# Performance work log

Measured on AMD Instinct MI355X. Metric: run time of the kernel, lower is better.

## Reference

```python
import jax, jax.numpy as jnp
import numpy as np
from jax import lax

B, S, H, V, J, K = 8, 512, 768, 35004, 30, 9
PAD = 0

def setup_inputs() -> dict:
    key = jax.random.key(0)
    ks = jax.random.split(key, 12)
    std = 0.02
    return {
        'x': jax.random.randint(ks[0], (B, S), 0, V),
        'decoder_input': jax.random.normal(ks[1], (B, J, H), jnp.float32),
        'encoder_output': jax.random.normal(ks[2], (B, S, H), jnp.float32),
        'hidden': jax.random.normal(ks[3], (1, B, H), jnp.float32),
        'teacher': jax.random.randint(ks[4], (B, J, K), 0, V),
        'max_len': K,
        'embed': jax.random.normal(ks[5], (V, H), jnp.float32) * std,
        'w_ih': jax.random.normal(ks[6], (3 * H, H), jnp.float32) * std,
        'w_hh': jax.random.normal(ks[7], (3 * H, H), jnp.float32) * std,
        'b_ih': jnp.zeros((3 * H,), jnp.float32),
        'b_hh': jnp.zeros((3 * H,), jnp.float32),
        'wg_w': jax.random.normal(ks[8], (1, 3 * H), jnp.float32) * std,
        'wg_b': jnp.zeros((1,), jnp.float32),
    }

def gru_cell(w, h, w_ih, w_hh, b_ih, b_hh):
    # PyTorch GRU gate order: reset, update, new
    gi = w @ w_ih.T + b_ih          # [B,3H]
    gh = h @ w_hh.T + b_hh          # [B,3H]
    ir, iz, inn = jnp.split(gi, 3, axis=-1)
    hr, hz, hn = jnp.split(gh, 3, axis=-1)
    r = jax.nn.sigmoid(ir + hr)
    z = jax.nn.sigmoid(iz + hz)
    n = jnp.tanh(inn + r * hn)
    return (1.0 - z) * n + z * h

def reference(x, decoder_input, encoder_output, hidden, teacher, max_len,
              embed, w_ih, w_hh, b_ih, b_hh, wg_w, wg_b):
    mask = (x == PAD)                      # [B,S]
    batch_ix = jnp.arange(x.shape[0])[:, None]

    def tok_step(carry, teach_t):
        w, h = carry                       # w,h: [B,H]; teach_t: [B]
        h = gru_cell(w, h, w_ih, w_hh, b_ih, b_hh)
        logits_hist = jnp.einsum('bsh,bh->bs', encoder_output, h)
        logits_hist = jnp.where(mask, -1e9, logits_hist)
        a_hist = jax.nn.softmax(logits_hist, axis=-1)          # [B,S]
        a_vocab = jax.nn.softmax(h @ embed.T, axis=-1)         # [B,V]
        context = jnp.einsum('bs,bsh->bh', a_hist, encoder_output)
        p_gen = jax.nn.sigmoid(
            jnp.concatenate([w, h, context], axis=-1) @ wg_w.T + wg_b)  # [B,1]
        p_ctx = jnp.zeros_like(a_vocab).at[batch_ix, x].add(a_hist)     # scatter_add pointer copy
        p_final = p_gen * a_vocab + (1.0 - p_gen) * p_ctx
        w_next = embed[teach_t]            # teacher forcing (dropout omitted: eval mode)
        return (w_next, h), p_final

    def slot_step(h, slot_in):
        w0, teach_j = slot_in              # w0: [B,H]; teach_j: [K,B]
        (_, h), p = lax.scan(tok_step, (w0, h), teach_j)
        return h, p                        # p: [K,B,V]

    h0 = hidden[0]                                      # [B,H]
    slots = jnp.swapaxes(decoder_input, 0, 1)           # [J,B,H]
    teach = jnp.transpose(teacher, (1, 2, 0))           # [J,K,B]
    _, outs = lax.scan(slot_step, h0, (slots, teach))   # [J,K,B,V]
    return jnp.transpose(outs, (2, 0, 1, 3))            # [B,J,K,V]
```

## Files before the change

### kernel.cpp

```cpp
#include <hip/hip_runtime.h>
#include <hip/hip_bf16.h>

typedef _Float16 f16;
typedef _Float16 f16x8 __attribute__((ext_vector_type(8)));
typedef _Float16 f16x4v __attribute__((ext_vector_type(4)));
typedef _Float16 h2 __attribute__((ext_vector_type(2)));
typedef float f32x4 __attribute__((ext_vector_type(4)));
typedef unsigned ui4v __attribute__((ext_vector_type(4)));
typedef unsigned long long ull;

#define B_ 8
#define S_ 512
#define H_ 768
#define V_ 35004
#define J_ 30
#define K_ 9
#define R_ 2160
#define H3 2304
#define VMT 17
#define VNT 274


__global__ void k_zero(int* p, int n) {
    int i = blockIdx.x * 256 + threadIdx.x;
    if (i < n) p[i] = 0;
}

__global__ void k_cast(const float* __restrict__ s, f16* __restrict__ d, long n) {
    for (long i = (long)blockIdx.x * 256 + threadIdx.x; i < n; i += (long)gridDim.x * 256)
        d[i] = (f16)s[i];
}

__global__ void k_build_wall(const float* __restrict__ emb, const float* __restrict__ dec,
                             const int* __restrict__ teacher, f16* __restrict__ Wall) {
    int r = blockIdx.x;
    int b = r / 270, s = r % 270, j = s / 9, t = s % 9;
    const float* src = (t == 0) ? dec + ((long)b * J_ + j) * H_
                                : emb + (long)teacher[((long)b * J_ + j) * K_ + (t - 1)] * H_;
    f16* dst = Wall + (long)r * H_;
    for (int c = threadIdx.x; c < H_; c += 256) dst[c] = (f16)src[c];
}

__global__ void k_init_h(const float* __restrict__ hidden, ull* __restrict__ hbuf) {
    int i = blockIdx.x * 256 + threadIdx.x;
    if (i < B_ * H_) {
        int b = i / H_, u = i % H_;
        hbuf[(long)b * 1536 + u] = (ull)__float_as_uint(hidden[i]);
    }
}

typedef const __attribute__((address_space(1))) unsigned GASU;
typedef __attribute__((address_space(3))) unsigned LASU;
__device__ __forceinline__ void gld16(const f16* g, f16* l) {
    __builtin_amdgcn_global_load_lds((GASU*)g, (LASU*)l, 16, 0, 0);
}

template <int MODE>
__global__ __launch_bounds__(256) void k_gemm(const f16* __restrict__ A, const f16* __restrict__ Bm,
                                              float* __restrict__ C, const float* __restrict__ bias,
                                              int M, int N, int K, long sA, long sB, long sC) {
    A += (long)blockIdx.z * sA;
    Bm += (long)blockIdx.z * sB;
    C += (long)blockIdx.z * sC;
    const int m0 = blockIdx.y * 128, n0 = blockIdx.x * 128;
    __shared__ f16 As[128 * 32];
    __shared__ f16 Bs[128 * 32];
    const int tid = threadIdx.x, lane = tid & 63, wave = tid >> 6;
    const int wm = wave >> 1, wn = wave & 1;
    const int fr = lane & 15, kg = lane >> 4;
    f32x4 acc[4][4] = {};
    const int idxu = wave * 128;
    const int i0 = idxu + lane, i1 = idxu + 64 + lane;
    const int r0 = i0 >> 2, k80 = i0 & 3;
    const int r1 = i1 >> 2, k81 = i1 & 3;
    int ga0 = m0 + r0; if (ga0 >= M) ga0 = M - 1;
    int ga1 = m0 + r1; if (ga1 >= M) ga1 = M - 1;
    int gb0 = n0 + r0; if (gb0 >= N) gb0 = N - 1;
    int gb1 = n0 + r1; if (gb1 >= N) gb1 = N - 1;
    const f16* pa0 = A + (long)ga0 * K + k80 * 8;
    const f16* pa1 = A + (long)ga1 * K + k81 * 8;
    const f16* pb0 = Bm + (long)gb0 * K + k80 * 8;
    const f16* pb1 = Bm + (long)gb1 * K + k81 * 8;
    for (int kt = 0; kt < K; kt += 32) {
        gld16(pa0 + kt, As + idxu * 8);
        gld16(pa1 + kt, As + idxu * 8 + 512);
        gld16(pb0 + kt, Bs + idxu * 8);
        gld16(pb1 + kt, Bs + idxu * 8 + 512);
        __syncthreads();
        f16x8 af[4], bf[4];
#pragma unroll
        for (int m = 0; m < 4; ++m) af[m] = *(const f16x8*)(As + (wm * 64 + m * 16 + fr) * 32 + kg * 8);
#pragma unroll
        for (int n = 0; n < 4; ++n) bf[n] = *(const f16x8*)(Bs + (wn * 64 + n * 16 + fr) * 32 + kg * 8);
#pragma unroll
        for (int m = 0; m < 4; ++m)
#pragma unroll
            for (int n = 0; n < 4; ++n)
                acc[m][n] = __builtin_amdgcn_mfma_f32_16x16x32_f16(af[m], bf[n], acc[m][n], 0, 0, 0);
        __syncthreads();
    }
    const int crow = m0 + wm * 64 + (lane >> 4) * 4;
    const int ccol = n0 + wn * 64 + fr;
#pragma unroll
    for (int n = 0; n < 4; ++n) {
        int col = ccol + n * 16;
        if (col >= N) continue;
        float bv = (MODE == 1) ? bias[col] : 0.f;
#pragma unroll
        for (int m = 0; m < 4; ++m) {
#pragma unroll
            for (int q = 0; q < 4; ++q) {
                int row = crow + m * 16 + q;
                if (row < M) C[(long)row * N + col] = acc[m][n][q] + bv;
            }
        }
    }
}

__global__ __launch_bounds__(256) void k_attn3(const f16* __restrict__ Ahi, const f16* __restrict__ Alo,
                                               const f16* __restrict__ Bhi, const f16* __restrict__ Blo,
                                               float* __restrict__ C, int M, int N, int K,
                                               long sA, long sB, long sC) {
    const long za = (long)blockIdx.z * sA, zb = (long)blockIdx.z * sB;
    C += (long)blockIdx.z * sC;
    const int m0 = blockIdx.y * 128, n0 = blockIdx.x * 128;
    __shared__ f16 As[128 * 32];
    __shared__ f16 Bs[128 * 32];
    const int tid = threadIdx.x, lane = tid & 63, wave = tid >> 6;
    const int wm = wave >> 1, wn = wave & 1;
    const int fr = lane & 15, kg = lane >> 4;
    f32x4 acc[4][4] = {};
    const int idxu = wave * 128;
    const int i0 = idxu + lane, i1 = idxu + 64 + lane;
    const int r0 = i0 >> 2, k80 = i0 & 3;
    const int r1 = i1 >> 2, k81 = i1 & 3;
    int ga0 = m0 + r0; if (ga0 >= M) ga0 = M - 1;
    int ga1 = m0 + r1; if (ga1 >= M) ga1 = M - 1;
    int gb0 = n0 + r0; if (gb0 >= N) gb0 = N - 1;
    int gb1 = n0 + r1; if (gb1 >= N) gb1 = N - 1;
    const long oa0 = (long)ga0 * K + k80 * 8, oa1 = (long)ga1 * K + k81 * 8;
    const long ob0 = (long)gb0 * K + k80 * 8, ob1 = (long)gb1 * K + k81 * 8;
    for (int ph = 0; ph < 3; ++ph) {
        const f16* Ap = (ph == 2 ? Alo : Ahi) + za;
        const f16* Bp = (ph == 1 ? Blo : Bhi) + zb;
        for (int kt = 0; kt < K; kt += 32) {
            gld16(Ap + oa0 + kt, As + idxu * 8);
            gld16(Ap + oa1 + kt, As + idxu * 8 + 512);
            gld16(Bp + ob0 + kt, Bs + idxu * 8);
            gld16(Bp + ob1 + kt, Bs + idxu * 8 + 512);
            __syncthreads();
            f16x8 af[4], bf[4];
#pragma unroll
            for (int m = 0; m < 4; ++m) af[m] = *(const f16x8*)(As + (wm * 64 + m * 16 + fr) * 32 + kg * 8);
#pragma unroll
            for (int n = 0; n < 4; ++n) bf[n] = *(const f16x8*)(Bs + (wn * 64 + n * 16 + fr) * 32 + kg * 8);
#pragma unroll
            for (int m = 0; m < 4; ++m)
#pragma unroll
                for (int n = 0; n < 4; ++n)
                    acc[m][n] = __builtin_amdgcn_mfma_f32_16x16x32_f16(af[m], bf[n], acc[m][n], 0, 0, 0);
            __syncthreads();
        }
    }
    const int crow = m0 + wm * 64 + (lane >> 4) * 4;
    const int ccol = n0 + wn * 64 + fr;
#pragma unroll
    for (int n = 0; n < 4; ++n) {
        int col = ccol + n * 16;
        if (col >= N) continue;
#pragma unroll
        for (int m = 0; m < 4; ++m) {
#pragma unroll
            for (int q = 0; q < 4; ++q) {
                int row = crow + m * 16 + q;
                if (row < M) C[(long)row * N + col] = acc[m][n][q];
            }
        }
    }
}

__global__ __launch_bounds__(256) void k_vocab(const f16* __restrict__ A, const f16* __restrict__ Bm,
                                               float* __restrict__ C, float* __restrict__ psum) {
    const int M = R_, N = V_, K = H_;
    const int nwg = VMT * VNT;
    int lin = blockIdx.x;
    int q8 = nwg / 8, r8 = nwg % 8;
    int xcd = lin & 7, idx = lin >> 3;
    int newlin = (xcd < r8) ? xcd * (q8 + 1) + idx : r8 * (q8 + 1) + (xcd - r8) * q8 + idx;
    int mt = newlin % VMT, nt = newlin / VMT;
    const int m0 = mt * 128, n0 = nt * 128;
    __shared__ f16 As[128 * 32];
    __shared__ f16 Bs[128 * 32];
    __shared__ float rpart[2][128];
    const int tid = threadIdx.x, lane = tid & 63, wave = tid >> 6;
    const int wm = wave >> 1, wn = wave & 1;
    const int fr = lane & 15, kg = lane >> 4;
    f32x4 acc[4][4] = {};
    const int idxu = wave * 128;
    const int i0 = idxu + lane, i1 = idxu + 64 + lane;
    const int r0 = i0 >> 2, k80 = i0 & 3;
    const int r1 = i1 >> 2, k81 = i1 & 3;
    int ga0 = m0 + r0; if (ga0 >= M) ga0 = M - 1;
    int ga1 = m0 + r1; if (ga1 >= M) ga1 = M - 1;
    int gb0 = n0 + r0; if (gb0 >= N) gb0 = N - 1;
    int gb1 = n0 + r1; if (gb1 >= N) gb1 = N - 1;
    const f16* pa0 = A + (long)ga0 * K + k80 * 8;
    const f16* pa1 = A + (long)ga1 * K + k81 * 8;
    const f16* pb0 = Bm + (long)gb0 * K + k80 * 8;
    const f16* pb1 = Bm + (long)gb1 * K + k81 * 8;
    for (int kt = 0; kt < K; kt += 32) {
        gld16(pa0 + kt, As + idxu * 8);
        gld16(pa1 + kt, As + idxu * 8 + 512);
        gld16(pb0 + kt, Bs + idxu * 8);
        gld16(pb1 + kt, Bs + idxu * 8 + 512);
        __syncthreads();
        f16x8 af[4], bf[4];
#pragma unroll
        for (int m = 0; m < 4; ++m) af[m] = *(const f16x8*)(As + (wm * 64 + m * 16 + fr) * 32 + kg * 8);
#pragma unroll
        for (int n = 0; n < 4; ++n) bf[n] = *(const f16x8*)(Bs + (wn * 64 + n * 16 + fr) * 32 + kg * 8);
#pragma unroll
        for (int m = 0; m < 4; ++m)
#pragma unroll
            for (int n = 0; n < 4; ++n)
                acc[m][n] = __builtin_amdgcn_mfma_f32_16x16x32_f16(af[m], bf[n], acc[m][n], 0, 0, 0);
        __syncthreads();
    }
    const int crow = m0 + wm * 64 + (lane >> 4) * 4;
    const int ccol = n0 + wn * 64 + fr;
    float rs[4][4];
#pragma unroll
    for (int m = 0; m < 4; ++m)
#pragma unroll
        for (int q = 0; q < 4; ++q) rs[m][q] = 0.f;
#pragma unroll
    for (int n = 0; n < 4; ++n) {
        int col = ccol + n * 16;
        if (col >= N) continue;
#pragma unroll
        for (int m = 0; m < 4; ++m) {
#pragma unroll
            for (int q = 0; q < 4; ++q) {
                int row = crow + m * 16 + q;
                if (row < M) {
                    float e = __expf(acc[m][n][q]);
                    C[(long)row * N + col] = e;
                    rs[m][q] += e;
                }
            }
        }
    }
#pragma unroll
    for (int m = 0; m < 4; ++m)
#pragma unroll
        for (int q = 0; q < 4; ++q) {
            float v = rs[m][q];
            v += __shfl_xor(v, 1);
            v += __shfl_xor(v, 2);
            v += __shfl_xor(v, 4);
            v += __shfl_xor(v, 8);
            rs[m][q] = v;
        }
    if ((lane & 15) == 0) {
#pragma unroll
        for (int m = 0; m < 4; ++m)
#pragma unroll
            for (int q = 0; q < 4; ++q)
                rpart[wn][wm * 64 + (lane >> 4) * 4 + m * 16 + q] = rs[m][q];
    }
    __syncthreads();
    if (tid < 128) {
        int row = m0 + tid;
        if (row < M) psum[(long)nt * M + row] = rpart[0][tid] + rpart[1][tid];
    }
}

__device__ __forceinline__ float fd2(unsigned hv, unsigned wv, float acc) {
#if __has_builtin(__builtin_amdgcn_fdot2)
    return __builtin_amdgcn_fdot2(__builtin_bit_cast(h2, hv), __builtin_bit_cast(h2, wv), acc, false);
#else
    h2 a = __builtin_bit_cast(h2, hv), b = __builtin_bit_cast(h2, wv);
    return acc + (float)a.x * (float)b.x + (float)a.y * (float)b.y;
#endif
}

__global__ __launch_bounds__(256, 1) void k_gru(const float* __restrict__ gi,
                                                const float* __restrict__ whh,
                                                const float* __restrict__ bhh,
                                                ull* hbuf,
                                                f16* __restrict__ Hhi, f16* __restrict__ Hlo,
                                                const float* __restrict__ emb, f16* __restrict__ emb16,
                                                const float* __restrict__ enc, f16* __restrict__ ehi,
                                                f16* __restrict__ elo, f16* __restrict__ encT) {
    __shared__ ui4v wsvu[9216];
    __shared__ __align__(16) f16 hsf[768];
    __shared__ float part[2][8][32][3];
    const int tid = threadIdx.x;
    if (blockIdx.x >= 192) {
        const long pt = (long)(blockIdx.x - 192) * 256 + tid;
        const long n4 = (long)V_ * H_ / 4;
        for (long i = pt; i < n4; i += 64 * 256) {
            f32x4 v = ((const f32x4*)emb)[i];
            f16x4v r = {(f16)v.x, (f16)v.y, (f16)v.z, (f16)v.w};
            ((f16x4v*)emb16)[i] = r;
        }
        const long n4e = (long)B_ * S_ * H_ / 4;
        for (long i = pt; i < n4e; i += 64 * 256) {
            f32x4 v = ((const f32x4*)enc)[i];
            f16 h0 = (f16)v.x, h1 = (f16)v.y, h2v = (f16)v.z, h3 = (f16)v.w;
            f16x4v hv = {h0, h1, h2v, h3};
            ((f16x4v*)ehi)[i] = hv;
            f16x4v lv = {(f16)(v.x - (float)h0), (f16)(v.y - (float)h1),
                         (f16)(v.z - (float)h2v), (f16)(v.w - (float)h3)};
            ((f16x4v*)elo)[i] = lv;
        }
        float* tl = (float*)wsvu;
        for (int t = blockIdx.x - 192; t < 8 * 8 * 12; t += 64) {
            int ht = t % 12, st = (t / 12) % 8, bb = t / 96;
            __syncthreads();
#pragma unroll
            for (int k = 0; k < 16; ++k) {
                int i = tid + k * 256;
                int sl = i >> 6, hl = i & 63;
                tl[sl * 65 + hl] = enc[((long)bb * S_ + st * 64 + sl) * H_ + ht * 64 + hl];
            }
            __syncthreads();
#pragma unroll
            for (int k = 0; k < 16; ++k) {
                int i = tid + k * 256;
                int hl = i >> 6, sl = i & 63;
                encT[((long)bb * H_ + ht * 64 + hl) * S_ + st * 64 + sl] = (f16)tl[sl * 65 + hl];
            }
        }
        return;
    }
    const int chain = blockIdx.x / 24;
    const int blk = blockIdx.x % 24;
    const int u0 = blk * 32;
    for (int idx = tid; idx < 9216; idx += 256) {
        int uu = idx & 31, k8 = (idx >> 5) % 96, g = idx / (96 * 32);
        const float* src = whh + (long)(g * H_ + u0 + uu) * H_ + k8 * 8;
        f32x4 a = *(const f32x4*)src;
        f32x4 b2 = *(const f32x4*)(src + 4);
        f16x8 pk = {(f16)a.x, (f16)a.y, (f16)a.z, (f16)a.w,
                    (f16)b2.x, (f16)b2.y, (f16)b2.z, (f16)b2.w};
        wsvu[idx] = __builtin_bit_cast(ui4v, pk);
    }
    float b_r = 0.f, b_z = 0.f, b_n = 0.f;
    if (tid < 32) {
        int c = u0 + tid;
        b_r = bhh[c];
        b_z = bhh[H_ + c];
        b_n = bhh[2 * H_ + c];
    }
    __syncthreads();
    const int u = tid & 31, q = tid >> 5, lane = tid & 63;
    const int pw = (tid >> 6) * 192 + lane;
    ui4v wreg[3][12];
#pragma unroll
    for (int g = 0; g < 3; ++g)
#pragma unroll
        for (int i = 0; i < 12; ++i)
            wreg[g][i] = wsvu[(g * 96 + q * 12 + i) * 32 + u];
    ull* base = hbuf + (long)chain * 1536;
    const bool fin = (tid < 32);
    float g0 = 0.f, g1 = 0.f, g2v = 0.f;
    if (fin) {
        const float* gp = gi + (long)chain * 270 * H3;
        int c = u0 + tid;
        g0 = gp[c];
        g1 = gp[H_ + c];
        g2v = gp[2 * H_ + c];
    }
    for (int s = 0; s < 270; ++s) {
        const ull* rb = base + (s & 1) * 768;
        ull* wb = base + ((s + 1) & 1) * 768;
        const unsigned want = (unsigned)s;
        ull v0, v1, v2, vh = 0;
        for (;;) {
            v0 = __hip_atomic_load(rb + pw, __ATOMIC_RELAXED, __HIP_MEMORY_SCOPE_AGENT);
            v1 = __hip_atomic_load(rb + pw + 64, __ATOMIC_RELAXED, __HIP_MEMORY_SCOPE_AGENT);
            v2 = __hip_atomic_load(rb + pw + 128, __ATOMIC_RELAXED, __HIP_MEMORY_SCOPE_AGENT);
            bool ok = ((unsigned)(v0 >> 32) == want) & ((unsigned)(v1 >> 32) == want) &
                      ((unsigned)(v2 >> 32) == want);
            if (fin) {
                vh = __hip_atomic_load(rb + u0 + tid, __ATOMIC_RELAXED, __HIP_MEMORY_SCOPE_AGENT);
                ok &= ((unsigned)(vh >> 32) == want);
            }
            if (ok) break;
        }
        hsf[pw] = (f16)__uint_as_float((unsigned)v0);
        hsf[pw + 64] = (f16)__uint_as_float((unsigned)v1);
        hsf[pw + 128] = (f16)__uint_as_float((unsigned)v2);
        __builtin_amdgcn_wave_barrier();
        float ar = 0.f, az = 0.f, an = 0.f;
#pragma unroll
        for (int i = 0; i < 12; ++i) {
            ui4v hv = *(const ui4v*)(&hsf[(q * 12 + i) * 8]);
            ui4v wr = wreg[0][i], wz = wreg[1][i], wn = wreg[2][i];
            ar = fd2(hv.x, wr.x, ar); ar = fd2(hv.y, wr.y, ar);
            ar = fd2(hv.z, wr.z, ar); ar = fd2(hv.w, wr.w, ar);
            az = fd2(hv.x, wz.x, az); az = fd2(hv.y, wz.y, az);
            az = fd2(hv.z, wz.z, az); az = fd2(hv.w, wz.w, az);
            an = fd2(hv.x, wn.x, an); an = fd2(hv.y, wn.y, an);
            an = fd2(hv.z, wn.z, an); an = fd2(hv.w, wn.w, an);
        }
        const int par = s & 1;
        part[par][q][u][0] = ar;
        part[par][q][u][1] = az;
        part[par][q][u][2] = an;
        __syncthreads();
        if (fin) {
            float gr = b_r, gz = b_z, gn = b_n;
#pragma unroll
            for (int qq = 0; qq < 8; ++qq) {
                gr += part[par][qq][tid][0];
                gz += part[par][qq][tid][1];
                gn += part[par][qq][tid][2];
            }
            float hold = __uint_as_float((unsigned)vh);
            float rg = 1.f / (1.f + expf(-(g0 + gr)));
            float zg = 1.f / (1.f + expf(-(g1 + gz)));
            float ng = tanhf(g2v + rg * gn);
            float hnew = (1.f - zg) * ng + zg * hold;
            int c = u0 + tid;
            ull wvv = ((ull)(unsigned)(s + 1) << 32) | (ull)__float_as_uint(hnew);
            __hip_atomic_store(wb + c, wvv, __ATOMIC_RELAXED, __HIP_MEMORY_SCOPE_AGENT);
            long row = (long)chain * 270 + s;
            f16 h16 = (f16)hnew;
            Hhi[row * H_ + c] = h16;
            Hlo[row * H_ + c] = (f16)(hnew - (float)h16);
            if (s < 269) {
                const float* gp = gi + ((long)chain * 270 + s + 1) * H3;
                g0 = gp[c];
                g1 = gp[H_ + c];
                g2v = gp[2 * H_ + c];
            }
        }
    }
}

__global__ __launch_bounds__(256) void k_attn_softmax(const float* __restrict__ lg,
                                                      const int* __restrict__ x, f16* __restrict__ ah) {
    __shared__ float red[256];
    int r = blockIdx.x, tid = threadIdx.x;
    int b = r / 270;
    const float* lr = lg + (long)r * S_;
    const int* xb = x + (long)b * S_;
    float v0 = lr[tid];
    if (xb[tid] == 0) v0 = -1e9f;
    float v1 = lr[tid + 256];
    if (xb[tid + 256] == 0) v1 = -1e9f;
    red[tid] = fmaxf(v0, v1);
    __syncthreads();
    for (int o = 128; o > 0; o >>= 1) {
        if (tid < o) red[tid] = fmaxf(red[tid], red[tid + o]);
        __syncthreads();
    }
    float m = red[0];
    __syncthreads();
    float e0 = __expf(v0 - m), e1 = __expf(v1 - m);
    red[tid] = e0 + e1;
    __syncthreads();
    for (int o = 128; o > 0; o >>= 1) {
        if (tid < o) red[tid] += red[tid + o];
        __syncthreads();
    }
    float inv = 1.f / red[0];
    ah[(long)r * S_ + tid] = (f16)(e0 * inv);
    ah[(long)r * S_ + tid + 256] = (f16)(e1 * inv);
}

__global__ __launch_bounds__(256) void k_pgen(const f16* __restrict__ Wall, const f16* __restrict__ Hhi,
                                              const f16* __restrict__ Hlo, const float* __restrict__ ctx,
                                              const float* __restrict__ wg, const float* __restrict__ wgb,
                                              float* __restrict__ pg) {
    __shared__ float red[256];
    int r = blockIdx.x, tid = threadIdx.x;
    float a = 0.f;
    for (int i = tid; i < H_; i += 256) {
        a += (float)Wall[(long)r * H_ + i] * wg[i];
        a += ((float)Hhi[(long)r * H_ + i] + (float)Hlo[(long)r * H_ + i]) * wg[H_ + i];
        a += ctx[(long)r * H_ + i] * wg[2 * H_ + i];
    }
    red[tid] = a;
    __syncthreads();
    for (int o = 128; o > 0; o >>= 1) {
        if (tid < o) red[tid] += red[tid + o];
        __syncthreads();
    }
    if (tid == 0) pg[r] = 1.f / (1.f + expf(-(red[0] + wgb[0])));
}

__global__ __launch_bounds__(256, 1) void k_fin3(float* __restrict__ out,
                                                 const float* __restrict__ psum,
                                                 const float* __restrict__ pg,
                                                 const f16* __restrict__ ah,
                                                 const int* __restrict__ x) {
    __shared__ float row[V_];
    __shared__ float red[256];
    const int r = blockIdx.x, tid = threadIdx.x;
    const int b = r / 270;
    float s = 0.f;
    for (int i = tid; i < VNT; i += 256) s += psum[(long)i * R_ + r];
    red[tid] = s;
    __syncthreads();
    for (int o = 128; o > 0; o >>= 1) {
        if (tid < o) red[tid] += red[tid + o];
        __syncthreads();
    }
    const float pgv = pg[r];
    const float scale = pgv / red[0];
    float* orow = out + (long)r * V_;
    for (int i = tid; i < V_ / 4; i += 256) {
        f32x4 v = ((const f32x4*)orow)[i];
        v.x *= scale;
        v.y *= scale;
        v.z *= scale;
        v.w *= scale;
        ((f32x4*)row)[i] = v;
    }
    __syncthreads();
    const float om = 1.f - pgv;
    for (int s2 = tid; s2 < S_; s2 += 256) {
        int xv = x[(long)b * S_ + s2];
        if (xv != 0) {
            float a = (float)ah[(long)r * S_ + s2];
            if (a != 0.f) atomicAdd(&row[xv], om * a);
        }
    }
    __syncthreads();
    for (int i = tid; i < V_ / 4; i += 256)
        ((f32x4*)orow)[i] = ((const f32x4*)row)[i];
}

extern "C" void kernel_launch(void* const* d_in, const int* in_sizes, int n_in, void* d_out,
                              int out_size, void* d_ws, size_t ws_size, hipStream_t stream) {
    (void)in_sizes; (void)n_in; (void)out_size; (void)ws_size;
    const int* x = (const int*)d_in[0];
    const float* dec = (const float*)d_in[1];
    const float* enc = (const float*)d_in[2];
    const float* hid = (const float*)d_in[3];
    const int* tea = (const int*)d_in[4];
    const float* emb = (const float*)d_in[6];
    const float* wih = (const float*)d_in[7];
    const float* whh = (const float*)d_in[8];
    const float* bih = (const float*)d_in[9];
    const float* bhh = (const float*)d_in[10];
    const float* wgw = (const float*)d_in[11];
    const float* wgb = (const float*)d_in[12];
    float* out = (float*)d_out;

    char* w = (char*)d_ws;
    size_t off = 0;
    auto alloc = [&](size_t bytes) {
        void* p = w + off;
        off = (off + bytes + 255) & ~(size_t)255;
        return p;
    };
    ull* hbuf = (ull*)alloc(8 * 1536 * 8);
    f16* Wall = (f16*)alloc((size_t)R_ * H_ * 2);
    f16* wih16 = (f16*)alloc((size_t)H3 * H_ * 2);
    float* giA = (float*)alloc((size_t)R_ * H3 * 4);
    f16* Hhi = (f16*)alloc((size_t)R_ * H_ * 2);
    f16* Hlo = (f16*)alloc((size_t)R_ * H_ * 2);
    f16* emb16 = (f16*)alloc((size_t)V_ * H_ * 2);
    f16* ehi = (f16*)alloc((size_t)B_ * S_ * H_ * 2);
    f16* elo = (f16*)alloc((size_t)B_ * S_ * H_ * 2);
    f16* encT = (f16*)alloc((size_t)B_ * H_ * S_ * 2);
    float* lgH = (float*)alloc((size_t)R_ * S_ * 4);
    f16* ah = (f16*)alloc((size_t)R_ * S_ * 2);
    float* ctx = (float*)alloc((size_t)R_ * H_ * 4);
    float* pg = (float*)alloc(R_ * 4);
    float* psum = (float*)alloc((size_t)VNT * R_ * 4);

    const int nH = 8 * 1536 * 2;
    k_zero<<<(nH + 255) / 256, 256, 0, stream>>>((int*)hbuf, nH);
    k_cast<<<512, 256, 0, stream>>>(wih, wih16, (long)H3 * H_);
    k_build_wall<<<R_, 256, 0, stream>>>(emb, dec, tea, Wall);
    k_init_h<<<24, 256, 0, stream>>>(hid, hbuf);

    {
        dim3 g(H3 / 128, (R_ + 127) / 128, 1);
        k_gemm<1><<<g, 256, 0, stream>>>(Wall, wih16, giA, bih, R_, H3, H_, 0, 0, 0);
    }
    k_gru<<<256, 256, 0, stream>>>(giA, whh, bhh, hbuf, Hhi, Hlo,
                                   emb, emb16, enc, ehi, elo, encT);

    {
        dim3 g(S_ / 128, 3, 8);
        k_attn3<<<g, 256, 0, stream>>>(Hhi, Hlo, ehi, elo, lgH, 270, S_, H_,
                                       270L * H_, (long)S_ * H_, 270L * S_);
    }
    k_attn_softmax<<<R_, 256, 0, stream>>>(lgH, x, ah);
    {
        dim3 g(H_ / 128, 3, 8);
        k_gemm<0><<<g, 256, 0, stream>>>(ah, encT, ctx, nullptr, 270, H_, S_, 270L * S_, (long)H_ * S_, 270L * H_);
    }
    k_pgen<<<R_, 256, 0, stream>>>(Wall, Hhi, Hlo, ctx, wgw, wgb, pg);

    k_vocab<<<VMT * VNT, 256, 0, stream>>>(Hhi, emb16, out, psum);
    k_fin3<<<R_, 256, 0, stream>>>(out, psum, pg, ah, x);
}
```

Measured before the change: 1.117 ms.

## Overlap vocab GEMM with GRU recurrence via progress flags and atomic tile queue

The 64 helper blocks of the GRU kernel, once the conversions are done, now pull vocab-GEMM tiles from a global atomic counter. Before each tile they wait on per-block progress flags until the needed hidden rows exist, which overlaps the vocab GEMM with the serial GRU recurrence. The GRU writes hidden states into a step-major f16 buffer so early M-tiles depend only on early steps, and the output rows are remapped to match. The later k_vocab launch finishes whatever tiles are left. The GRU gate math also switches to fast __expf and an exp-based tanh, which adds spin-wait polling and costs some precision.

```diff
diff --git a/kernel.cpp b/kernel.cpp
--- a/kernel.cpp
+++ b/kernel.cpp
@@ -19,6 +19,9 @@
 #define H3 2304
 #define VMT 17
 #define VNT 274
+#define NTILE (VMT * VNT)
+
+#define CTL_INTS 512
 
 
 __global__ void k_zero(int* p, int n) {
@@ -179,20 +182,13 @@
     }
 }
 
-__global__ __launch_bounds__(256) void k_vocab(const f16* __restrict__ A, const f16* __restrict__ Bm,
-                                               float* __restrict__ C, float* __restrict__ psum) {
+__device__ __forceinline__ void vocab_tile(int mt, int nt, const f16* __restrict__ A,
+                                           const f16* __restrict__ Bm, float* __restrict__ C,
+                                           float* __restrict__ psum, f16* As, f16* Bs,
+                                           float* rpart, int tid) {
     const int M = R_, N = V_, K = H_;
-    const int nwg = VMT * VNT;
-    int lin = blockIdx.x;
-    int q8 = nwg / 8, r8 = nwg % 8;
-    int xcd = lin & 7, idx = lin >> 3;
-    int newlin = (xcd < r8) ? xcd * (q8 + 1) + idx : r8 * (q8 + 1) + (xcd - r8) * q8 + idx;
-    int mt = newlin % VMT, nt = newlin / VMT;
     const int m0 = mt * 128, n0 = nt * 128;
-    __shared__ f16 As[128 * 32];
-    __shared__ f16 Bs[128 * 32];
-    __shared__ float rpart[2][128];
-    const int tid = threadIdx.x, lane = tid & 63, wave = tid >> 6;
+    const int lane = tid & 63, wave = tid >> 6;
     const int wm = wave >> 1, wn = wave & 1;
     const int fr = lane & 15, kg = lane >> 4;
     f32x4 acc[4][4] = {};
@@ -243,8 +239,9 @@
             for (int q = 0; q < 4; ++q) {
                 int row = crow + m * 16 + q;
                 if (row < M) {
+                    int orow = (row & 7) * 270 + (row >> 3);
                     float e = __expf(acc[m][n][q]);
-                    C[(long)row * N + col] = e;
+                    C[(long)orow * N + col] = e;
                     rs[m][q] += e;
                 }
             }
@@ -266,13 +263,31 @@
         for (int m = 0; m < 4; ++m)
 #pragma unroll
             for (int q = 0; q < 4; ++q)
-                rpart[wn][wm * 64 + (lane >> 4) * 4 + m * 16 + q] = rs[m][q];
+                rpart[wn * 128 + wm * 64 + (lane >> 4) * 4 + m * 16 + q] = rs[m][q];
     }
     __syncthreads();
     if (tid < 128) {
         int row = m0 + tid;
-        if (row < M) psum[(long)nt * M + row] = rpart[0][tid] + rpart[1][tid];
-    }
+        if (row < M) {
+            int orow = (row & 7) * 270 + (row >> 3);
+            psum[(long)nt * M + orow] = rpart[tid] + rpart[128 + tid];
+        }
+    }
+}
+
+__global__ __launch_bounds__(256) void k_vocab(const f16* __restrict__ Hs, const f16* __restrict__ emb16,
+                                               float* __restrict__ out, float* __restrict__ psum,
+                                               int* ctl) {
+    __shared__ f16 As[128 * 32];
+    __shared__ f16 Bs[128 * 32];
+    __shared__ float rpart[256];
+    __shared__ int q_s;
+    if (threadIdx.x == 0)
+        q_s = __hip_atomic_fetch_add(ctl, 1, __ATOMIC_RELAXED, __HIP_MEMORY_SCOPE_AGENT);
+    __syncthreads();
+    int q = q_s;
+    if (q >= NTILE) return;
+    vocab_tile(q / VNT, q % VNT, Hs, emb16, out, psum, As, Bs, rpart, threadIdx.x);
 }
 
 __device__ __forceinline__ float fd2(unsigned hv, unsigned wv, float acc) {
@@ -289,20 +304,26 @@
                                                 const float* __restrict__ bhh,
                                                 ull* hbuf,
                                                 f16* __restrict__ Hhi, f16* __restrict__ Hlo,
+                                                f16* __restrict__ Hs,
                                                 const float* __restrict__ emb, f16* __restrict__ emb16,
                                                 const float* __restrict__ enc, f16* __restrict__ ehi,
-                                                f16* __restrict__ elo, f16* __restrict__ encT) {
+                                                f16* __restrict__ elo, f16* __restrict__ encT,
+                                                float* __restrict__ out, float* __restrict__ psum,
+                                                int* ctl) {
     __shared__ ui4v wsvu[9216];
     __shared__ __align__(16) f16 hsf[768];
     __shared__ float part[2][8][32][3];
+    __shared__ int q_s;
     const int tid = threadIdx.x;
+    int* prog = ctl + 256;
     if (blockIdx.x >= 192) {
         const long pt = (long)(blockIdx.x - 192) * 256 + tid;
         const long n4 = (long)V_ * H_ / 4;
         for (long i = pt; i < n4; i += 64 * 256) {
             f32x4 v = ((const f32x4*)emb)[i];
             f16x4v r = {(f16)v.x, (f16)v.y, (f16)v.z, (f16)v.w};
-            ((f16x4v*)emb16)[i] = r;
+            __hip_atomic_store((ull*)emb16 + i, __builtin_bit_cast(ull, r),
+                               __ATOMIC_RELAXED, __HIP_MEMORY_SCOPE_AGENT);
         }
         const long n4e = (long)B_ * S_ * H_ / 4;
         for (long i = pt; i < n4e; i += 64 * 256) {
@@ -331,6 +352,46 @@
                 int hl = i >> 6, sl = i & 63;
                 encT[((long)bb * H_ + ht * 64 + hl) * S_ + st * 64 + sl] = (f16)tl[sl * 65 + hl];
             }
+        }
+        if (tid == 0) {
+            asm volatile("s_waitcnt vmcnt(0)" ::: "memory");
+            __hip_atomic_fetch_add(ctl + 32, 1, __ATOMIC_RELAXED, __HIP_MEMORY_SCOPE_AGENT);
+            while (__hip_atomic_load(ctl + 32, __ATOMIC_RELAXED, __HIP_MEMORY_SCOPE_AGENT) < 64)
+                __builtin_amdgcn_s_sleep(8);
+            __builtin_amdgcn_fence(__ATOMIC_ACQUIRE, "agent");
+        }
+        __syncthreads();
+        f16* Asp = (f16*)wsvu;
+        f16* Bsp = Asp + 128 * 32;
+        float* rpp = (float*)(Bsp + 128 * 32);
+        for (;;) {
+            if (tid == 0) {
+                int q = -1;
+                if (__hip_atomic_load(ctl + 64, __ATOMIC_RELAXED, __HIP_MEMORY_SCOPE_AGENT) < 192) {
+                    q = __hip_atomic_fetch_add(ctl, 1, __ATOMIC_RELAXED, __HIP_MEMORY_SCOPE_AGENT);
+                    if (q >= NTILE) q = -1;
+                }
+                if (q >= 0) {
+                    int mt = q / VNT;
+                    int need = ((mt * 128 + 127) >> 3) + 1;
+                    for (;;) {
+                        int mn = 1 << 30;
+                        for (int i2 = 0; i2 < 192; ++i2) {
+                            int v = __hip_atomic_load(prog + i2, __ATOMIC_RELAXED, __HIP_MEMORY_SCOPE_AGENT);
+                            mn = v < mn ? v : mn;
+                        }
+                        if (mn >= need) break;
+                        __builtin_amdgcn_s_sleep(16);
+                    }
+                    __builtin_amdgcn_fence(__ATOMIC_ACQUIRE, "agent");
+                }
+                q_s = q;
+            }
+            __syncthreads();
+            int q = q_s;
+            if (q < 0) break;
+            vocab_tile(q / VNT, q % VNT, Hs, emb16, out, psum, Asp, Bsp, rpp, tid);
+            __syncthreads();
         }
         return;
     }
@@ -419,9 +480,11 @@
                 gn += part[par][qq][tid][2];
             }
             float hold = __uint_as_float((unsigned)vh);
-            float rg = 1.f / (1.f + expf(-(g0 + gr)));
-            float zg = 1.f / (1.f + expf(-(g1 + gz)));
-            float ng = tanhf(g2v + rg * gn);
+            float rg = 1.f / (1.f + __expf(-(g0 + gr)));
+            float zg = 1.f / (1.f + __expf(-(g1 + gz)));
+            float xa = g2v + rg * gn;
+            float e2 = __expf(-2.f * xa);
+            float ng = (1.f - e2) / (1.f + e2);
             float hnew = (1.f - zg) * ng + zg * hold;
             int c = u0 + tid;
             ull wvv = ((ull)(unsigned)(s + 1) << 32) | (ull)__float_as_uint(hnew);
@@ -430,6 +493,17 @@
             f16 h16 = (f16)hnew;
             Hhi[row * H_ + c] = h16;
             Hlo[row * H_ + c] = (f16)(hnew - (float)h16);
+            unsigned hb = (unsigned)__builtin_bit_cast(unsigned short, h16);
+            unsigned up2 = (unsigned)__shfl_down((int)hb, 1);
+            if (!(tid & 1)) {
+                long sidx = ((long)s * 8 + chain) * H_ + c;
+                __hip_atomic_store((unsigned*)Hs + (sidx >> 1), hb | (up2 << 16),
+                                   __ATOMIC_RELAXED, __HIP_MEMORY_SCOPE_AGENT);
+            }
+            asm volatile("s_waitcnt vmcnt(0)" ::: "memory");
+            if (tid == 0)
+                __hip_atomic_store(prog + chain * 24 + blk, s + 1,
+                                   __ATOMIC_RELAXED, __HIP_MEMORY_SCOPE_AGENT);
             if (s < 269) {
                 const float* gp = gi + ((long)chain * 270 + s + 1) * H3;
                 g0 = gp[c];
@@ -438,6 +512,8 @@
             }
         }
     }
+    if (tid == 0)
+        __hip_atomic_fetch_add(ctl + 64, 1, __ATOMIC_RELAXED, __HIP_MEMORY_SCOPE_AGENT);
 }
 
 __global__ __launch_bounds__(256) void k_attn_softmax(const float* __restrict__ lg,
@@ -558,12 +634,14 @@
         off = (off + bytes + 255) & ~(size_t)255;
         return p;
     };
+    int* ctl = (int*)alloc(CTL_INTS * 4);
     ull* hbuf = (ull*)alloc(8 * 1536 * 8);
     f16* Wall = (f16*)alloc((size_t)R_ * H_ * 2);
     f16* wih16 = (f16*)alloc((size_t)H3 * H_ * 2);
     float* giA = (float*)alloc((size_t)R_ * H3 * 4);
     f16* Hhi = (f16*)alloc((size_t)R_ * H_ * 2);
     f16* Hlo = (f16*)alloc((size_t)R_ * H_ * 2);
+    f16* Hs = (f16*)alloc((size_t)R_ * H_ * 2);
     f16* emb16 = (f16*)alloc((size_t)V_ * H_ * 2);
     f16* ehi = (f16*)alloc((size_t)B_ * S_ * H_ * 2);
     f16* elo = (f16*)alloc((size_t)B_ * S_ * H_ * 2);
@@ -574,8 +652,8 @@
     float* pg = (float*)alloc(R_ * 4);
     float* psum = (float*)alloc((size_t)VNT * R_ * 4);
 
-    const int nH = 8 * 1536 * 2;
-    k_zero<<<(nH + 255) / 256, 256, 0, stream>>>((int*)hbuf, nH);
+    const int nZ = CTL_INTS + 8 * 1536 * 2;
+    k_zero<<<(nZ + 255) / 256, 256, 0, stream>>>(ctl, nZ);
     k_cast<<<512, 256, 0, stream>>>(wih, wih16, (long)H3 * H_);
     k_build_wall<<<R_, 256, 0, stream>>>(emb, dec, tea, Wall);
     k_init_h<<<24, 256, 0, stream>>>(hid, hbuf);
@@ -584,8 +662,8 @@
         dim3 g(H3 / 128, (R_ + 127) / 128, 1);
         k_gemm<1><<<g, 256, 0, stream>>>(Wall, wih16, giA, bih, R_, H3, H_, 0, 0, 0);
     }
-    k_gru<<<256, 256, 0, stream>>>(giA, whh, bhh, hbuf, Hhi, Hlo,
-                                   emb, emb16, enc, ehi, elo, encT);
+    k_gru<<<256, 256, 0, stream>>>(giA, whh, bhh, hbuf, Hhi, Hlo, Hs,
+                                   emb, emb16, enc, ehi, elo, encT, out, psum, ctl);
 
     {
         dim3 g(S_ / 128, 3, 8);
@@ -599,6 +677,6 @@
     }
     k_pgen<<<R_, 256, 0, stream>>>(Wall, Hhi, Hlo, ctx, wgw, wgb, pg);
 
-    k_vocab<<<VMT * VNT, 256, 0, stream>>>(Hhi, emb16, out, psum);
+    k_vocab<<<NTILE, 256, 0, stream>>>(Hs, emb16, out, psum, ctl);
     k_fin3<<<R_, 256, 0, stream>>>(out, psum, pg, ah, x);
 }
```

New measurement: 1.224 ms. +9.6%, slower.

## Fuse prep kernels and parallelize GRU gate reduction across all threads

Applied to the files above, without the earlier changes.

Merges the zero, cast and Wall-build launches into one prep kernel, and moves the hbuf zeroing into k_init_h. In the serial GRU step loop, the gate reduction over the 8 partial sums now runs across all 256 threads with xor shuffles instead of 32 threads each summing 8 LDS entries. The part array is padded to avoid bank conflicts. expf/tanhf are replaced by fast __expf-based forms, which shortens the per-step critical path at a small accuracy cost.

```diff
diff --git a/kernel.cpp b/kernel.cpp
--- a/kernel.cpp
+++ b/kernel.cpp
@@ -19,26 +19,24 @@
 #define H3 2304
 #define VMT 17
 #define VNT 274
-
-
-__global__ void k_zero(int* p, int n) {
-    int i = blockIdx.x * 256 + threadIdx.x;
-    if (i < n) p[i] = 0;
-}
-
-__global__ void k_cast(const float* __restrict__ s, f16* __restrict__ d, long n) {
-    for (long i = (long)blockIdx.x * 256 + threadIdx.x; i < n; i += (long)gridDim.x * 256)
-        d[i] = (f16)s[i];
-}
-
-__global__ void k_build_wall(const float* __restrict__ emb, const float* __restrict__ dec,
-                             const int* __restrict__ teacher, f16* __restrict__ Wall) {
+#define CASTB 864
+
+
+__global__ void k_prep(const float* __restrict__ emb, const float* __restrict__ dec,
+                       const int* __restrict__ teacher, f16* __restrict__ Wall,
+                       const float* __restrict__ wih, f16* __restrict__ wih16) {
     int r = blockIdx.x;
-    int b = r / 270, s = r % 270, j = s / 9, t = s % 9;
-    const float* src = (t == 0) ? dec + ((long)b * J_ + j) * H_
-                                : emb + (long)teacher[((long)b * J_ + j) * K_ + (t - 1)] * H_;
-    f16* dst = Wall + (long)r * H_;
-    for (int c = threadIdx.x; c < H_; c += 256) dst[c] = (f16)src[c];
+    if (r < R_) {
+        int b = r / 270, s = r % 270, j = s / 9, t = s % 9;
+        const float* src = (t == 0) ? dec + ((long)b * J_ + j) * H_
+                                    : emb + (long)teacher[((long)b * J_ + j) * K_ + (t - 1)] * H_;
+        f16* dst = Wall + (long)r * H_;
+        for (int c = threadIdx.x; c < H_; c += 256) dst[c] = (f16)src[c];
+    } else {
+        const long n = (long)H3 * H_;
+        for (long i = (long)(r - R_) * 256 + threadIdx.x; i < n; i += (long)CASTB * 256)
+            wih16[i] = (f16)wih[i];
+    }
 }
 
 __global__ void k_init_h(const float* __restrict__ hidden, ull* __restrict__ hbuf) {
@@ -46,6 +44,7 @@
     if (i < B_ * H_) {
         int b = i / H_, u = i % H_;
         hbuf[(long)b * 1536 + u] = (ull)__float_as_uint(hidden[i]);
+        hbuf[(long)b * 1536 + 768 + u] = 0;
     }
 }
 
@@ -294,7 +293,7 @@
                                                 f16* __restrict__ elo, f16* __restrict__ encT) {
     __shared__ ui4v wsvu[9216];
     __shared__ __align__(16) f16 hsf[768];
-    __shared__ float part[2][8][32][3];
+    __shared__ float part[2][8][33][3];
     const int tid = threadIdx.x;
     if (blockIdx.x >= 192) {
         const long pt = (long)(blockIdx.x - 192) * 256 + tid;
@@ -346,9 +345,12 @@
                     (f16)b2.x, (f16)b2.y, (f16)b2.z, (f16)b2.w};
         wsvu[idx] = __builtin_bit_cast(ui4v, pk);
     }
+    const bool own = (tid & 7) == 0;
+    const int unit = tid >> 3;
+    const int jl = tid & 7;
     float b_r = 0.f, b_z = 0.f, b_n = 0.f;
-    if (tid < 32) {
-        int c = u0 + tid;
+    if (own) {
+        int c = u0 + unit;
         b_r = bhh[c];
         b_z = bhh[H_ + c];
         b_n = bhh[2 * H_ + c];
@@ -363,11 +365,10 @@
         for (int i = 0; i < 12; ++i)
             wreg[g][i] = wsvu[(g * 96 + q * 12 + i) * 32 + u];
     ull* base = hbuf + (long)chain * 1536;
-    const bool fin = (tid < 32);
     float g0 = 0.f, g1 = 0.f, g2v = 0.f;
-    if (fin) {
+    if (own) {
         const float* gp = gi + (long)chain * 270 * H3;
-        int c = u0 + tid;
+        int c = u0 + unit;
         g0 = gp[c];
         g1 = gp[H_ + c];
         g2v = gp[2 * H_ + c];
@@ -383,8 +384,8 @@
             v2 = __hip_atomic_load(rb + pw + 128, __ATOMIC_RELAXED, __HIP_MEMORY_SCOPE_AGENT);
             bool ok = ((unsigned)(v0 >> 32) == want) & ((unsigned)(v1 >> 32) == want) &
                       ((unsigned)(v2 >> 32) == want);
-            if (fin) {
-                vh = __hip_atomic_load(rb + u0 + tid, __ATOMIC_RELAXED, __HIP_MEMORY_SCOPE_AGENT);
+            if (own) {
+                vh = __hip_atomic_load(rb + u0 + unit, __ATOMIC_RELAXED, __HIP_MEMORY_SCOPE_AGENT);
                 ok &= ((unsigned)(vh >> 32) == want);
             }
             if (ok) break;
@@ -410,20 +411,22 @@
         part[par][q][u][1] = az;
         part[par][q][u][2] = an;
         __syncthreads();
-        if (fin) {
-            float gr = b_r, gz = b_z, gn = b_n;
-#pragma unroll
-            for (int qq = 0; qq < 8; ++qq) {
-                gr += part[par][qq][tid][0];
-                gz += part[par][qq][tid][1];
-                gn += part[par][qq][tid][2];
-            }
+        float gr = part[par][jl][unit][0];
+        float gz = part[par][jl][unit][1];
+        float gn = part[par][jl][unit][2];
+        gr += __shfl_xor(gr, 1); gz += __shfl_xor(gz, 1); gn += __shfl_xor(gn, 1);
+        gr += __shfl_xor(gr, 2); gz += __shfl_xor(gz, 2); gn += __shfl_xor(gn, 2);
+        gr += __shfl_xor(gr, 4); gz += __shfl_xor(gz, 4); gn += __shfl_xor(gn, 4);
+        if (own) {
+            gr += b_r; gz += b_z; gn += b_n;
             float hold = __uint_as_float((unsigned)vh);
-            float rg = 1.f / (1.f + expf(-(g0 + gr)));
-            float zg = 1.f / (1.f + expf(-(g1 + gz)));
-            float ng = tanhf(g2v + rg * gn);
+            float rg = 1.f / (1.f + __expf(-(g0 + gr)));
+            float zg = 1.f / (1.f + __expf(-(g1 + gz)));
+            float xa = g2v + rg * gn;
+            float e2 = __expf(-2.f * xa);
+            float ng = (1.f - e2) / (1.f + e2);
             float hnew = (1.f - zg) * ng + zg * hold;
-            int c = u0 + tid;
+            int c = u0 + unit;
             ull wvv = ((ull)(unsigned)(s + 1) << 32) | (ull)__float_as_uint(hnew);
             __hip_atomic_store(wb + c, wvv, __ATOMIC_RELAXED, __HIP_MEMORY_SCOPE_AGENT);
             long row = (long)chain * 270 + s;
@@ -574,11 +577,8 @@
     float* pg = (float*)alloc(R_ * 4);
     float* psum = (float*)alloc((size_t)VNT * R_ * 4);
 
-    const int nH = 8 * 1536 * 2;
-    k_zero<<<(nH + 255) / 256, 256, 0, stream>>>((int*)hbuf, nH);
-    k_cast<<<512, 256, 0, stream>>>(wih, wih16, (long)H3 * H_);
-    k_build_wall<<<R_, 256, 0, stream>>>(emb, dec, tea, Wall);
     k_init_h<<<24, 256, 0, stream>>>(hid, hbuf);
+    k_prep<<<R_ + CASTB, 256, 0, stream>>>(emb, dec, tea, Wall, wih, wih16);
 
     {
         dim3 g(H3 / 128, (R_ + 127) / 128, 1);
```

Result: no change. 1.138 ms (+1.8%).
